# Kernel tuning notes

Hardware: AMD Instinct MI355X
Metric: run time of the kernel (lower is better)

The kernel has to match this reference:

```python
import jax, jax.numpy as jnp
import numpy as np

B, T, C = 4, 2048, 1024
H = 16
HD = C // H  # 64


def setup_inputs() -> dict:
    key = jax.random.key(0)
    k1, k2, k3 = jax.random.split(key, 3)
    x = jax.random.normal(k1, (B, T, C), dtype=jnp.float32)
    w_qkv = jax.random.normal(k2, (C, 3 * C), dtype=jnp.float32) * (C ** -0.5)
    b_qkv = jnp.zeros((3 * C,), dtype=jnp.float32)
    w_proj = jax.random.normal(k3, (C, C), dtype=jnp.float32) * (C ** -0.5)
    b_proj = jnp.zeros((C,), dtype=jnp.float32)
    return {"x": x, "w_qkv": w_qkv, "b_qkv": b_qkv, "w_proj": w_proj, "b_proj": b_proj}


def reference(x, w_qkv, b_qkv, w_proj, b_proj):
    b, t, c = x.shape
    qkv = x @ w_qkv + b_qkv  # [b,t,3c]
    q, k, v = jnp.split(qkv, 3, axis=-1)

    def split_heads(z):
        return z.reshape(b, t, H, HD).transpose(0, 2, 1, 3)  # [b,h,t,hd]

    q, k, v = split_heads(q), split_heads(k), split_heads(v)
    scale = HD ** -0.5
    att = jnp.einsum("bhqd,bhkd->bhqk", q, k) * scale  # [b,h,t,t]
    causal = jnp.tril(jnp.ones((t, t), dtype=bool))
    att = jnp.where(causal[None, None], att, -jnp.inf)
    att = jax.nn.softmax(att, axis=-1)
    y = jnp.einsum("bhqk,bhkd->bhqd", att, v)  # [b,h,t,hd]
    y = y.transpose(0, 2, 1, 3).reshape(b, t, c)
    return y @ w_proj + b_proj
```

## Files before the change

kernel.cpp:

```cpp
#include <hip/hip_runtime.h>

typedef unsigned short ushort_t;
typedef __attribute__((ext_vector_type(8))) short bf16x8;
typedef __attribute__((ext_vector_type(4))) float f32x4;
typedef __attribute__((ext_vector_type(16))) float f32x16;
typedef __attribute__((ext_vector_type(4))) unsigned short u16x4;
typedef __attribute__((ext_vector_type(2))) int i32x2;

__device__ __forceinline__ ushort_t f2bf(float f) {
  unsigned int u = __float_as_uint(f);
  u += 0x7FFFu + ((u >> 16) & 1u);
  return (ushort_t)(u >> 16);
}

__device__ __forceinline__ int cvt_pk_bf16(float lo, float hi) {
  int r;
  asm("v_cvt_pk_bf16_f32 %0, %1, %2" : "=v"(r) : "v"(lo), "v"(hi));
  return r;
}

__device__ __forceinline__ void gload16(const void* g, void* l) {
  __builtin_amdgcn_global_load_lds((__attribute__((address_space(1))) void*)g,
                                   (__attribute__((address_space(3))) void*)l, 16, 0, 0);
}


__global__ __launch_bounds__(256) void cast_kernel(const float* __restrict__ in,
                                                   ushort_t* __restrict__ out, int n4) {
  int i = blockIdx.x * 256 + threadIdx.x;
  if (i >= n4) return;
  float4 v = ((const float4*)in)[i];
  u16x4 o = {f2bf(v.x), f2bf(v.y), f2bf(v.z), f2bf(v.w)};
  *(u16x4*)(out + (size_t)i * 4) = o;
}

__global__ __launch_bounds__(256) void transpose_cast(const float* __restrict__ in,
                                                      ushort_t* __restrict__ out, int R, int C) {
  __shared__ float tile[64][65];
  int c0 = blockIdx.x * 64, r0 = blockIdx.y * 64;
  int tid = threadIdx.x;
  int lr = tid >> 2, q = tid & 3;
  const float* ip = in + (size_t)(r0 + lr) * C + c0 + q * 16;
#pragma unroll
  for (int j = 0; j < 16; ++j) tile[lr][q * 16 + j] = ip[j];
  __syncthreads();
  int oc = tid >> 2;
  ushort_t* op = out + (size_t)(c0 + oc) * R + r0 + q * 16;
#pragma unroll
  for (int j = 0; j < 16; ++j) op[j] = f2bf(tile[q * 16 + j][oc]);
}


template <int MODE>
__global__ __launch_bounds__(256, 4) void gemm_kernel(
    const ushort_t* __restrict__ A, const ushort_t* __restrict__ Bt,
    const float* __restrict__ bias, float* __restrict__ OutF,
    ushort_t* __restrict__ Qh, ushort_t* __restrict__ Kh, ushort_t* __restrict__ Vt,
    int K, int NTN) {
  __shared__ __align__(16) char smem[32768];
  const int nwg = gridDim.x;
  const int cpx = nwg >> 3;
  const int logical = (blockIdx.x & 7) * cpx + (blockIdx.x >> 3);
  const int m0 = (logical / NTN) * 128;
  const int n0 = (logical % NTN) * 128;
  const int tid = threadIdx.x;
  const int l = tid & 63;
  const int l4 = l >> 4;
  const int w = tid >> 6;
  const int wr = (w >> 1) * 64;
  const int wc = (w & 1) * 64;

  const f32x4 z = {0.f, 0.f, 0.f, 0.f};
  f32x4 acc[4][4];
#pragma unroll
  for (int i = 0; i < 4; ++i)
#pragma unroll
    for (int j = 0; j < 4; ++j) acc[i][j] = z;

  const int ldsw = (tid & ~63) * 16;

  for (int kt = 0; kt < K; kt += 64) {
    __syncthreads();
#pragma unroll
    for (int i = 0; i < 4; ++i) {
      int c = tid + i * 256;
      int row = c >> 3, g = c & 7;
      int gc = (g ^ (row & 7)) << 3;
      gload16(A + (size_t)(m0 + row) * K + kt + gc, smem + i * 4096 + ldsw);
      gload16(Bt + (size_t)(n0 + row) * K + kt + gc, smem + 16384 + i * 4096 + ldsw);
    }
    __syncthreads();
    bf16x8 af[4][2], bf[4][2];
#pragma unroll
    for (int i = 0; i < 4; ++i) {
      int ra = wr + i * 16 + (l & 15);
      const char* rb = smem + ra * 128;
      af[i][0] = *(const bf16x8*)(rb + (((l4) ^ (ra & 7)) << 4));
      af[i][1] = *(const bf16x8*)(rb + (((4 + l4) ^ (ra & 7)) << 4));
      int rbr = wc + i * 16 + (l & 15);
      const char* bb = smem + 16384 + rbr * 128;
      bf[i][0] = *(const bf16x8*)(bb + (((l4) ^ (rbr & 7)) << 4));
      bf[i][1] = *(const bf16x8*)(bb + (((4 + l4) ^ (rbr & 7)) << 4));
    }
#pragma unroll
    for (int mi = 0; mi < 4; ++mi)
#pragma unroll
      for (int ni = 0; ni < 4; ++ni) {
        acc[mi][ni] = __builtin_amdgcn_mfma_f32_16x16x32_bf16(af[mi][0], bf[ni][0],
                                                              acc[mi][ni], 0, 0, 0);
        acc[mi][ni] = __builtin_amdgcn_mfma_f32_16x16x32_bf16(af[mi][1], bf[ni][1],
                                                              acc[mi][ni], 0, 0, 0);
      }
  }

  if (MODE == 0) {
    const int which = n0 >> 10;
    if (which < 2) {
      ushort_t* outp = which == 0 ? Qh : Kh;
#pragma unroll
      for (int ni = 0; ni < 4; ++ni) {
        int col = n0 + wc + ni * 16 + (l & 15);
        float bv = bias[col];
        int cc = col & 1023;
        int h = cc >> 6, d = cc & 63;
#pragma unroll
        for (int mi = 0; mi < 4; ++mi) {
#pragma unroll
          for (int r = 0; r < 4; ++r) {
            int grow = m0 + wr + mi * 16 + l4 * 4 + r;
            int bb = grow >> 11, t = grow & 2047;
            outp[((size_t)(bb * 16 + h) * 2048 + t) * 64 + d] = f2bf(acc[mi][ni][r] + bv);
          }
        }
      }
    } else {
#pragma unroll
      for (int ni = 0; ni < 4; ++ni) {
        int col = n0 + wc + ni * 16 + (l & 15);
        float bv = bias[col];
        int cc = col & 1023;
        int h = cc >> 6, d = cc & 63;
#pragma unroll
        for (int mi = 0; mi < 4; ++mi) {
          int grow0 = m0 + wr + mi * 16 + l4 * 4;
          int bb = grow0 >> 11, tt = grow0 & 2047;
          u16x4 pk;
#pragma unroll
          for (int r = 0; r < 4; ++r) pk[r] = f2bf(acc[mi][ni][r] + bv);
          *(u16x4*)(Vt + ((size_t)(bb * 16 + h) * 64 + d) * 2048 + tt) = pk;
        }
      }
    }
  } else {
#pragma unroll
    for (int ni = 0; ni < 4; ++ni) {
      int col = n0 + wc + ni * 16 + (l & 15);
      float bv = bias[col];
#pragma unroll
      for (int mi = 0; mi < 4; ++mi) {
#pragma unroll
        for (int r = 0; r < 4; ++r) {
          int grow = m0 + wr + mi * 16 + l4 * 4 + r;
          OutF[(size_t)grow * 1024 + col] = acc[mi][ni][r] + bv;
        }
      }
    }
  }
}


__global__ __launch_bounds__(512, 4) void attn_kernel(
    const ushort_t* __restrict__ Qh, const ushort_t* __restrict__ Kh,
    const ushort_t* __restrict__ Vt, ushort_t* __restrict__ Y) {
  __shared__ __align__(16) char smem[32768];
  const int id  = blockIdx.x;
  const int x   = id & 7;
  const int g   = id >> 3;
  const int bh  = x * 8 + (g & 7);
  const int qs  = 7 - (g >> 3);
  const int q0  = qs * 256;
  const int tid = threadIdx.x;
  const int l   = tid & 63;
  const int w   = tid >> 6;
  const int q31 = l & 31;
  const int h   = l >> 5;
  const int qw  = q0 + w * 32;
  const int qg  = qw + q31;
  const size_t bK = (size_t)bh * (2048 * 64);
  const float SC = 0.18033688f;

  const int srow = tid >> 3;
  const int scol = (((tid & 7) << 4) ^ ((srow & 7) << 4)) >> 1;
  const ushort_t* ksrc = Kh + bK + (size_t)srow * 64 + scol;
  const ushort_t* vsrc = Vt + (size_t)bh * (64 * 2048) + (size_t)srow * 2048 + scol;
  char* const dstK = smem + w * 1024;
  char* const dstV = smem + 8192 + w * 1024;

  const int fsw = ((q31 & 7) << 4);
  const int kfb = q31 * 128;
  bf16x8 qf[4];
  {
    const ushort_t* qp = Qh + bK + (size_t)qg * 64 + h * 8;
#pragma unroll
    for (int i = 0; i < 4; ++i) qf[i] = *(const bf16x8*)(qp + i * 16);
  }

  const f32x16 fz = {0.f,0.f,0.f,0.f,0.f,0.f,0.f,0.f,0.f,0.f,0.f,0.f,0.f,0.f,0.f,0.f};
  f32x16 o0 = fz, o1 = fz;
  float lsum = 0.f;
  const int nkv = qs * 4 + 4;

  gload16(ksrc, dstK);
  gload16(vsrc + 0, dstV);
  __syncthreads();

  int cur = 0;
  for (int t = 0; t < nkv; ++t) {
    const int kv0 = t * 64;
    if (t + 1 < nkv) {
      gload16(ksrc + (size_t)(kv0 + 64) * 64, dstK + (cur ^ 1) * 16384);
      gload16(vsrc + kv0 + 64, dstV + (cur ^ 1) * 16384);
    }
    if (kv0 <= qw + 31) {
      const char* kb = smem + cur * 16384;
      const char* vb = kb + 8192;
      f32x16 s0 = fz, s1 = fz;
      __builtin_amdgcn_s_setprio(1);
#pragma unroll
      for (int i = 0; i < 4; ++i) {
        bf16x8 k0 = *(const bf16x8*)(kb + kfb + ((i * 32 + h * 16) ^ fsw));
        bf16x8 k1 = *(const bf16x8*)(kb + 4096 + kfb + ((i * 32 + h * 16) ^ fsw));
        s0 = __builtin_amdgcn_mfma_f32_32x32x16_bf16(k0, qf[i], s0, 0, 0, 0);
        s1 = __builtin_amdgcn_mfma_f32_32x32x16_bf16(k1, qf[i], s1, 0, 0, 0);
      }
      __builtin_amdgcn_s_setprio(0);

      if (kv0 + 63 > qw) {
#pragma unroll
        for (int r = 0; r < 16; ++r) {
          const int crow = (r & 3) + 8 * (r >> 2) + 4 * h;
          if (kv0 + crow > qg) s0[r] = -3e38f;
          if (kv0 + 32 + crow > qg) s1[r] = -3e38f;
        }
      }

      float rs = 0.f;
#pragma unroll
      for (int r = 0; r < 16; ++r) {
        float p0 = __builtin_amdgcn_exp2f(__builtin_fmaf(s0[r], SC, -8.f));
        float p1 = __builtin_amdgcn_exp2f(__builtin_fmaf(s1[r], SC, -8.f));
        s0[r] = p0; s1[r] = p1;
        rs += p0 + p1;
      }
      rs += __shfl_xor(rs, 32);
      lsum += rs;

      bf16x8 pa[4];
#pragma unroll
      for (int sl = 0; sl < 2; ++sl) {
        int wd[8];
#pragma unroll
        for (int i = 0; i < 8; ++i)
          wd[i] = sl ? cvt_pk_bf16(s1[2 * i], s1[2 * i + 1])
                     : cvt_pk_bf16(s0[2 * i], s0[2 * i + 1]);
#pragma unroll
        for (int pp = 0; pp < 2; ++pp) {
          i32x2 r0 = __builtin_amdgcn_permlane32_swap(wd[pp * 4 + 0], wd[pp * 4 + 2], false, false);
          i32x2 r1 = __builtin_amdgcn_permlane32_swap(wd[pp * 4 + 1], wd[pp * 4 + 3], false, false);
          union { int i[4]; bf16x8 v; } u;
          u.i[0] = r0[0]; u.i[1] = r1[0]; u.i[2] = r0[1]; u.i[3] = r1[1];
          pa[sl * 2 + pp] = u.v;
        }
      }

      __builtin_amdgcn_s_setprio(1);
#pragma unroll
      for (int ks = 0; ks < 4; ++ks) {
        bf16x8 va0 = *(const bf16x8*)(vb + kfb + ((ks * 32 + h * 16) ^ fsw));
        bf16x8 va1 = *(const bf16x8*)(vb + 4096 + kfb + ((ks * 32 + h * 16) ^ fsw));
        o0 = __builtin_amdgcn_mfma_f32_32x32x16_bf16(va0, pa[ks], o0, 0, 0, 0);
        o1 = __builtin_amdgcn_mfma_f32_32x32x16_bf16(va1, pa[ks], o1, 0, 0, 0);
      }
      __builtin_amdgcn_s_setprio(0);
    }
    __syncthreads();
    cur ^= 1;
  }

  const float inv = 1.f / lsum;
  const int b = bh >> 4, hh = bh & 15;
  ushort_t* yp = Y + ((size_t)(b * 2048 + qg)) * 1024 + hh * 64;
#pragma unroll
  for (int grp = 0; grp < 2; ++grp) {
#pragma unroll
    for (int rg = 0; rg < 4; ++rg) {
      int d0 = grp * 32 + rg * 8 + h * 4;
      u16x4 pk;
#pragma unroll
      for (int j = 0; j < 4; ++j)
        pk[j] = f2bf((grp ? o1[rg * 4 + j] : o0[rg * 4 + j]) * inv);
      *(u16x4*)(yp + d0) = pk;
    }
  }
}


extern "C" void kernel_launch(void* const* d_in, const int* in_sizes, int n_in,
                              void* d_out, int out_size, void* d_ws, size_t ws_size,
                              hipStream_t stream) {
  const float* x      = (const float*)d_in[0];
  const float* w_qkv  = (const float*)d_in[1];
  const float* b_qkv  = (const float*)d_in[2];
  const float* w_proj = (const float*)d_in[3];
  const float* b_proj = (const float*)d_in[4];
  float* out = (float*)d_out;

  char* ws = (char*)d_ws;
  ushort_t* xb = (ushort_t*)(ws + 0);
  ushort_t* Wq = (ushort_t*)(ws + (16u << 20));
  ushort_t* Wp = (ushort_t*)(ws + (22u << 20));
  ushort_t* Qh = (ushort_t*)(ws + (24u << 20));
  ushort_t* Kh = (ushort_t*)(ws + (40u << 20));
  ushort_t* Vt = (ushort_t*)(ws + (56u << 20));

  cast_kernel<<<8192, 256, 0, stream>>>(x, xb, 2097152);
  transpose_cast<<<dim3(48, 16), 256, 0, stream>>>(w_qkv, Wq, 1024, 3072);
  transpose_cast<<<dim3(16, 16), 256, 0, stream>>>(w_proj, Wp, 1024, 1024);

  gemm_kernel<0><<<1536, 256, 0, stream>>>(xb, Wq, b_qkv, nullptr, Qh, Kh, Vt, 1024, 24);
  attn_kernel<<<512, 512, 0, stream>>>(Qh, Kh, Vt, xb );
  gemm_kernel<1><<<512, 256, 0, stream>>>(xb, Wp, b_proj, out, nullptr, nullptr, nullptr, 1024, 8);
}
```

Before: 165.9 us.

## Double-buffer GEMM LDS tiles and overlap prefetch with MFMA via vmcnt waits

The GEMM kernel now uses two 32 KB LDS stages and issues the next K-tile's global-to-LDS loads before computing the current one. It waits with partial vmcnt counts instead of draining all loads at a full __syncthreads. The attention kernel's existing double buffer switches to the same explicit vmcnt-plus-s_barrier scheme so the next KV tile's loads stay in flight. The intent is to hide global load latency behind MFMA work, at the cost of doubling GEMM LDS and lowering the occupancy bound from 4 to 2 blocks per CU.

```diff
diff --git a/kernel.cpp b/kernel.cpp
--- a/kernel.cpp
+++ b/kernel.cpp
@@ -52,12 +52,12 @@
 
 
 template <int MODE>
-__global__ __launch_bounds__(256, 4) void gemm_kernel(
+__global__ __launch_bounds__(256, 2) void gemm_kernel(
     const ushort_t* __restrict__ A, const ushort_t* __restrict__ Bt,
     const float* __restrict__ bias, float* __restrict__ OutF,
     ushort_t* __restrict__ Qh, ushort_t* __restrict__ Kh, ushort_t* __restrict__ Vt,
     int K, int NTN) {
-  __shared__ __align__(16) char smem[32768];
+  __shared__ __align__(16) char smem[65536];
   const int nwg = gridDim.x;
   const int cpx = nwg >> 3;
   const int logical = (blockIdx.x & 7) * cpx + (blockIdx.x >> 3);
@@ -79,29 +79,46 @@
 
   const int ldsw = (tid & ~63) * 16;
 
-  for (int kt = 0; kt < K; kt += 64) {
-    __syncthreads();
-#pragma unroll
-    for (int i = 0; i < 4; ++i) {
-      int c = tid + i * 256;
-      int row = c >> 3, g = c & 7;
-      int gc = (g ^ (row & 7)) << 3;
-      gload16(A + (size_t)(m0 + row) * K + kt + gc, smem + i * 4096 + ldsw);
-      gload16(Bt + (size_t)(n0 + row) * K + kt + gc, smem + 16384 + i * 4096 + ldsw);
-    }
-    __syncthreads();
+#define STAGE(KT, TB)                                                               \
+  do {                                                                              \
+    _Pragma("unroll")                                                               \
+    for (int i = 0; i < 4; ++i) {                                                   \
+      int c = tid + i * 256;                                                        \
+      int row = c >> 3, g = c & 7;                                                  \
+      int gc = (g ^ (row & 7)) << 3;                                                \
+      gload16(A + (size_t)(m0 + row) * K + (KT) + gc,                               \
+              smem + (TB) * 32768 + i * 4096 + ldsw);                               \
+      gload16(Bt + (size_t)(n0 + row) * K + (KT) + gc,                              \
+              smem + (TB) * 32768 + 16384 + i * 4096 + ldsw);                       \
+    }                                                                               \
+  } while (0)
+
+  STAGE(0, 0);
+  const int NT = K >> 6;
+  for (int t = 0; t < NT; ++t) {
+    if (t + 1 < NT) {
+      STAGE((t + 1) * 64, (t + 1) & 1);
+      asm volatile("s_waitcnt vmcnt(8)" ::: "memory");
+    } else {
+      asm volatile("s_waitcnt vmcnt(0)" ::: "memory");
+    }
+    __builtin_amdgcn_s_barrier();
+    __builtin_amdgcn_sched_barrier(0);
+    const char* Ab = smem + (t & 1) * 32768;
+    const char* Bb = Ab + 16384;
     bf16x8 af[4][2], bf[4][2];
 #pragma unroll
     for (int i = 0; i < 4; ++i) {
       int ra = wr + i * 16 + (l & 15);
-      const char* rb = smem + ra * 128;
+      const char* rb = Ab + ra * 128;
       af[i][0] = *(const bf16x8*)(rb + (((l4) ^ (ra & 7)) << 4));
       af[i][1] = *(const bf16x8*)(rb + (((4 + l4) ^ (ra & 7)) << 4));
       int rbr = wc + i * 16 + (l & 15);
-      const char* bb = smem + 16384 + rbr * 128;
+      const char* bb = Bb + rbr * 128;
       bf[i][0] = *(const bf16x8*)(bb + (((l4) ^ (rbr & 7)) << 4));
       bf[i][1] = *(const bf16x8*)(bb + (((4 + l4) ^ (rbr & 7)) << 4));
     }
+    __builtin_amdgcn_s_setprio(1);
 #pragma unroll
     for (int mi = 0; mi < 4; ++mi)
 #pragma unroll
@@ -111,7 +128,11 @@
         acc[mi][ni] = __builtin_amdgcn_mfma_f32_16x16x32_bf16(af[mi][1], bf[ni][1],
                                                               acc[mi][ni], 0, 0, 0);
       }
-  }
+    __builtin_amdgcn_s_setprio(0);
+    __builtin_amdgcn_sched_barrier(0);
+    __builtin_amdgcn_s_barrier();
+  }
+#undef STAGE
 
   if (MODE == 0) {
     const int which = n0 >> 10;
@@ -212,17 +233,20 @@
 
   gload16(ksrc, dstK);
   gload16(vsrc + 0, dstV);
-  __syncthreads();
-
-  int cur = 0;
+
   for (int t = 0; t < nkv; ++t) {
     const int kv0 = t * 64;
     if (t + 1 < nkv) {
-      gload16(ksrc + (size_t)(kv0 + 64) * 64, dstK + (cur ^ 1) * 16384);
-      gload16(vsrc + kv0 + 64, dstV + (cur ^ 1) * 16384);
-    }
+      gload16(ksrc + (size_t)(kv0 + 64) * 64, dstK + ((t + 1) & 1) * 16384);
+      gload16(vsrc + kv0 + 64, dstV + ((t + 1) & 1) * 16384);
+      asm volatile("s_waitcnt vmcnt(2)" ::: "memory");
+    } else {
+      asm volatile("s_waitcnt vmcnt(0)" ::: "memory");
+    }
+    __builtin_amdgcn_s_barrier();
+    __builtin_amdgcn_sched_barrier(0);
     if (kv0 <= qw + 31) {
-      const char* kb = smem + cur * 16384;
+      const char* kb = smem + (t & 1) * 16384;
       const char* vb = kb + 8192;
       f32x16 s0 = fz, s1 = fz;
       __builtin_amdgcn_s_setprio(1);
@@ -283,8 +307,8 @@
       }
       __builtin_amdgcn_s_setprio(0);
     }
-    __syncthreads();
-    cur ^= 1;
+    __builtin_amdgcn_sched_barrier(0);
+    __builtin_amdgcn_s_barrier();
   }
 
   const float inv = 1.f / lsum;
```

After: 160.9 us. 3.0% less time.

## Merge weight transpose launches and use explicit vmcnt waits in attention loop

Applied to the files above, without the earlier changes.

Merges the two weight transpose-cast launches into one kernel that picks its source by block index, removing a launch. In the attention kernel, the full __syncthreads calls around the double-buffered K/V prefetch become explicit s_waitcnt vmcnt plus raw s_barrier. Each iteration now waits only for the current tile's loads while the next tile's async loads stay in flight, so prefetch overlaps compute. This depends on the vmcnt counts matching the number of outstanding global_load_lds ops, which is fragile if the compiler emits other vector memory loads.

```diff
diff --git a/kernel.cpp b/kernel.cpp
--- a/kernel.cpp
+++ b/kernel.cpp
@@ -34,10 +34,17 @@
   *(u16x4*)(out + (size_t)i * 4) = o;
 }
 
-__global__ __launch_bounds__(256) void transpose_cast(const float* __restrict__ in,
-                                                      ushort_t* __restrict__ out, int R, int C) {
+__global__ __launch_bounds__(256) void transpose_cast2(const float* __restrict__ inA,
+                                                       ushort_t* __restrict__ outA,
+                                                       const float* __restrict__ inB,
+                                                       ushort_t* __restrict__ outB) {
   __shared__ float tile[64][65];
-  int c0 = blockIdx.x * 64, r0 = blockIdx.y * 64;
+  const int bx = blockIdx.x;
+  const float* in = bx < 48 ? inA : inB;
+  ushort_t* out = bx < 48 ? outA : outB;
+  const int C = bx < 48 ? 3072 : 1024;
+  const int cb = bx < 48 ? bx : bx - 48;
+  int c0 = cb * 64, r0 = blockIdx.y * 64;
   int tid = threadIdx.x;
   int lr = tid >> 2, q = tid & 3;
   const float* ip = in + (size_t)(r0 + lr) * C + c0 + q * 16;
@@ -45,7 +52,7 @@
   for (int j = 0; j < 16; ++j) tile[lr][q * 16 + j] = ip[j];
   __syncthreads();
   int oc = tid >> 2;
-  ushort_t* op = out + (size_t)(c0 + oc) * R + r0 + q * 16;
+  ushort_t* op = out + (size_t)(c0 + oc) * 1024 + r0 + q * 16;
 #pragma unroll
   for (int j = 0; j < 16; ++j) op[j] = f2bf(tile[q * 16 + j][oc]);
 }
@@ -212,17 +219,20 @@
 
   gload16(ksrc, dstK);
   gload16(vsrc + 0, dstV);
-  __syncthreads();
-
-  int cur = 0;
+
   for (int t = 0; t < nkv; ++t) {
     const int kv0 = t * 64;
     if (t + 1 < nkv) {
-      gload16(ksrc + (size_t)(kv0 + 64) * 64, dstK + (cur ^ 1) * 16384);
-      gload16(vsrc + kv0 + 64, dstV + (cur ^ 1) * 16384);
-    }
+      gload16(ksrc + (size_t)(kv0 + 64) * 64, dstK + ((t + 1) & 1) * 16384);
+      gload16(vsrc + kv0 + 64, dstV + ((t + 1) & 1) * 16384);
+      asm volatile("s_waitcnt vmcnt(2)" ::: "memory");
+    } else {
+      asm volatile("s_waitcnt vmcnt(0)" ::: "memory");
+    }
+    __builtin_amdgcn_s_barrier();
+    __builtin_amdgcn_sched_barrier(0);
     if (kv0 <= qw + 31) {
-      const char* kb = smem + cur * 16384;
+      const char* kb = smem + (t & 1) * 16384;
       const char* vb = kb + 8192;
       f32x16 s0 = fz, s1 = fz;
       __builtin_amdgcn_s_setprio(1);
@@ -283,8 +293,8 @@
       }
       __builtin_amdgcn_s_setprio(0);
     }
-    __syncthreads();
-    cur ^= 1;
+    __builtin_amdgcn_sched_barrier(0);
+    __builtin_amdgcn_s_barrier();
   }
 
   const float inv = 1.f / lsum;
@@ -324,8 +334,7 @@
   ushort_t* Vt = (ushort_t*)(ws + (56u << 20));
 
   cast_kernel<<<8192, 256, 0, stream>>>(x, xb, 2097152);
-  transpose_cast<<<dim3(48, 16), 256, 0, stream>>>(w_qkv, Wq, 1024, 3072);
-  transpose_cast<<<dim3(16, 16), 256, 0, stream>>>(w_proj, Wp, 1024, 1024);
+  transpose_cast2<<<dim3(64, 16), 256, 0, stream>>>(w_qkv, Wq, w_proj, Wp);
 
   gemm_kernel<0><<<1536, 256, 0, stream>>>(xb, Wq, b_qkv, nullptr, Qh, Kh, Vt, 1024, 24);
   attn_kernel<<<512, 512, 0, stream>>>(Qh, Kh, Vt, xb );
```

New measurement: 164.6 us. Within noise of the previous version (-0.8%).
